# Performance work log

Hardware: AMD Instinct MI355X
Metric: run time of the kernel (lower is better)

## Reference

```python
import jax, jax.numpy as jnp
import numpy as np

N = 50000          # nodes
E = 800000         # edges per relation per prop step (avg degree 16)
NNZ = 1600000      # total sparse feature entries (32 per node)
IN_DIM = 20000     # feature vocab (EmbeddingBag rows)
H_DIM = 128        # hidden dim
OUT_DIM = 256      # GO label dim
HEADS = 1
LN_EPS = 1e-5


def _xn(k, shape, gain=1.0):
    fan_in, fan_out = shape[0], shape[-1]
    std = gain * np.sqrt(2.0 / (fan_in + fan_out))
    return std * jax.random.normal(k, shape, dtype=jnp.float32)


def setup_inputs() -> dict:
    key = jax.random.key(0)
    ks = jax.random.split(key, 32)
    d = {}
    d['emb_indices'] = jax.random.randint(ks[0], (NNZ,), 0, IN_DIM)
    d['emb_offsets'] = jnp.arange(N + 1) * (NNZ // N)  # include_last_offset=True
    d['emb_weights'] = jax.random.uniform(ks[1], (NNZ,), dtype=jnp.float32)
    d['y'] = jax.random.uniform(ks[2], (N, OUT_DIM), dtype=jnp.float32)
    d['flag'] = jax.random.randint(ks[3], (N,), 0, 2).astype(bool)
    for i, name in enumerate(['src_p1', 'dst_p1', 'src_s1', 'dst_s1',
                              'src_p2', 'dst_p2', 'src_s2', 'dst_s2']):
        d[name] = jax.random.randint(ks[4 + i], (E,), 0, N)
    g = np.sqrt(2.0)  # relu gain
    d['embed_W'] = _xn(ks[12], (IN_DIM, H_DIM))
    d['embed_b'] = jnp.zeros((H_DIM,), jnp.float32)
    d['mlp_W1'] = _xn(ks[13], (H_DIM, H_DIM)); d['mlp_b1'] = jnp.zeros((H_DIM,), jnp.float32)
    d['ln1_g'] = jnp.ones((H_DIM,), jnp.float32); d['ln1_b'] = jnp.zeros((H_DIM,), jnp.float32)
    d['mlp_W2'] = _xn(ks[14], (H_DIM, H_DIM)); d['mlp_b2'] = jnp.zeros((H_DIM,), jnp.float32)
    d['ln2_g'] = jnp.ones((H_DIM,), jnp.float32); d['ln2_b'] = jnp.zeros((H_DIM,), jnp.float32)
    d['Wsrc1'] = _xn(ks[15], (H_DIM, HEADS * H_DIM), g); d['bsrc1'] = jnp.zeros((HEADS * H_DIM,), jnp.float32)
    d['attn1'] = _xn(ks[16], (1, HEADS, H_DIM), g)
    d['Wsrc2'] = _xn(ks[17], (H_DIM, HEADS * H_DIM), g); d['bsrc2'] = jnp.zeros((HEADS * H_DIM,), jnp.float32)
    d['attn2'] = _xn(ks[18], (1, HEADS, H_DIM), g)
    d['out_W'] = _xn(ks[19], (H_DIM, OUT_DIM)); d['out_b'] = jnp.zeros((OUT_DIM,), jnp.float32)
    return d


def _layernorm(x, g, b):
    mu = jnp.mean(x, axis=-1, keepdims=True)
    var = jnp.mean((x - mu) ** 2, axis=-1, keepdims=True)
    return (x - mu) * jax.lax.rsqrt(var + LN_EPS) * g + b


def _edge_softmax(s, dst, n):
    # per-destination-node softmax over incoming edges, per head. s: (E, H)
    m = jax.ops.segment_max(s, dst, num_segments=n)
    ex = jnp.exp(s - m[dst])
    den = jax.ops.segment_sum(ex, dst, num_segments=n)
    return ex / den[dst]


def _gat(x, src, dst, W, b, attn, n):
    # block semantics: feat_dst = feat_src[:n_dst] (fc_dst unused in DGL block path)
    f = (x @ W + b).reshape(n, HEADS, -1)            # (N, H, F)
    e = jax.nn.leaky_relu(f[src] + f[dst], 0.2)       # u_add_v, (E, H, F)
    s = jnp.sum(e * attn, axis=-1)                    # (E, H)
    a = _edge_softmax(s, dst, n)                      # (E, H)
    rst = jax.ops.segment_sum(f[src] * a[:, :, None], dst, num_segments=n)  # (N,H,F)
    rst = rst + x[:, None, :]  # Identity residual (heads=1, in_dim == out_feats)
    return rst.mean(axis=1), a.mean(axis=1)           # (N, F), (E,)


def _prop(x, y, flag, src_p, dst_p, src_s, dst_s, W, b, attn, n):
    h_p, a_p = _gat(x, src_p, dst_p, W, b, attn, n)
    h_s, a_s = _gat(x, src_s, dst_s, W, b, attn, n)
    h = jax.nn.elu(h_p + h_s)
    # label propagation: u_mul_e with the (averaged) attention coefficients
    y_i = jax.ops.segment_sum(y[src_p] * a_p[:, None], dst_p, num_segments=n)
    y_s = jax.ops.segment_sum(y[src_s] * a_s[:, None], dst_s, num_segments=n)
    yh = y_i + y_s
    yh = yh / jnp.maximum(jnp.linalg.norm(yh, axis=1, keepdims=True), 1e-12)  # F.normalize
    yh = jnp.where(flag[:, None], y, yh)  # y_hat[dst_flag] = y0
    return h, yh


def reference(emb_indices, emb_offsets, emb_weights, y, flag,
              src_p1, dst_p1, src_s1, dst_s1, src_p2, dst_p2, src_s2, dst_s2,
              embed_W, embed_b, mlp_W1, mlp_b1, ln1_g, ln1_b,
              mlp_W2, mlp_b2, ln2_g, ln2_b,
              Wsrc1, bsrc1, attn1, Wsrc2, bsrc2, attn2, out_W, out_b):
    n = emb_offsets.shape[0] - 1
    nnz = emb_indices.shape[0]
    # EmbeddingBag(mode='sum', per_sample_weights, include_last_offset=True)
    seg = jnp.searchsorted(emb_offsets, jnp.arange(nnz), side='right') - 1
    h = jax.ops.segment_sum(embed_W[emb_indices] * emb_weights[:, None], seg, num_segments=n)
    h = jax.nn.relu(h + embed_b)
    # MLP: (Linear -> LayerNorm -> ReLU) x 2, dropout=0 (eval)
    h = jax.nn.relu(_layernorm(h @ mlp_W1 + mlp_b1, ln1_g, ln1_b))
    h = jax.nn.relu(_layernorm(h @ mlp_W2 + mlp_b2, ln2_g, ln2_b))
    h, yh = _prop(h, y, flag, src_p1, dst_p1, src_s1, dst_s1, Wsrc1, bsrc1, attn1, n)
    h, yh = _prop(h, yh, flag, src_p2, dst_p2, src_s2, dst_s2, Wsrc2, bsrc2, attn2, n)
    return h @ out_W + out_b, yh
```

## Files before the change

kernel.cpp:

```cpp
#include <hip/hip_runtime.h>
#include <hip/hip_bf16.h>

using bf16 = __hip_bfloat16;

#define HD 128
#define OD 256
#define NPASS 8

__device__ __forceinline__ float bl(unsigned lo){ return __uint_as_float(lo << 16); }
__device__ __forceinline__ float bh(unsigned u){ return __uint_as_float(u & 0xffff0000u); }

__device__ __forceinline__ void loadw4(const float* W, size_t off, float* w){
  float4 v = *(const float4*)(W + off); w[0]=v.x; w[1]=v.y; w[2]=v.z; w[3]=v.w;
}
__device__ __forceinline__ void loadw4(const bf16* W, size_t off, float* w){
  uint2 v = *(const uint2*)(W + off);
  w[0]=bl(v.x); w[1]=bh(v.x); w[2]=bl(v.y); w[3]=bh(v.y);
}

__global__ void k_detect(const void* __restrict__ w, int* __restrict__ dflag){
  if (threadIdx.x != 0 || blockIdx.x != 0) return;
  const bf16* p = (const bf16*)w;
  int f32 = 0;
  for (int i = 0; i < 128; ++i){
    float v = (float)p[i];
    if (!(v >= -0.001f && v <= 1.001f)) { f32 = 1; break; }
  }
  *dflag = f32;
}

__global__ void k_pack(const void* __restrict__ src, bf16* __restrict__ dst,
                       int n, const int* __restrict__ dflag){
  int i = blockIdx.x*blockDim.x + threadIdx.x;
  if (i >= n) return;
  float v = *dflag ? ((const float*)src)[i] : (float)((const bf16*)src)[i];
  dst[i] = (bf16)v;
}

__global__ void k_zero(int* __restrict__ p, int n){
  int i = blockIdx.x*blockDim.x + threadIdx.x;
  if (i < n) p[i] = 0;
}
__global__ void k_count4(const int* __restrict__ d0, const int* __restrict__ d1,
                         const int* __restrict__ d2, const int* __restrict__ d3,
                         int e0, int e1, int e2, int e3,
                         int* __restrict__ deg4, int N){
  int r = blockIdx.y;
  const int* dst = (r==0)?d0:(r==1)?d1:(r==2)?d2:d3;
  int E = (r==0)?e0:(r==1)?e1:(r==2)?e2:e3;
  int e = blockIdx.x*blockDim.x + threadIdx.x;
  if (e < E) atomicAdd(&deg4[r*N + dst[e]], 1);
}
__global__ void k_scan4(const int* __restrict__ deg4, int* __restrict__ rs4,
                        int* __restrict__ cur4, int N){
  const int T = 1024;
  __shared__ int lds[T];
  int r = blockIdx.x;
  const int* deg = deg4 + (size_t)r*N;
  int* rs  = rs4 + (size_t)r*(N+1);
  int* cur = cur4 + (size_t)r*N;
  int t = threadIdx.x;
  int chunk = (N + T - 1) / T;
  int a = t*chunk, b = min(N, a + chunk);
  int s = 0;
  for (int i = a; i < b; ++i) s += deg[i];
  lds[t] = s; __syncthreads();
  for (int o = 1; o < T; o <<= 1){
    int x = (t >= o) ? lds[t-o] : 0;
    __syncthreads();
    lds[t] += x;
    __syncthreads();
  }
  int run = (t > 0) ? lds[t-1] : 0;
  for (int i = a; i < b; ++i){ rs[i] = run; cur[i] = run; run += deg[i]; }
  if (t == T-1) rs[N] = lds[T-1];
}
__global__ void k_scatter4(const int* __restrict__ s0, const int* __restrict__ d0,
                           const int* __restrict__ s1, const int* __restrict__ d1,
                           const int* __restrict__ s2, const int* __restrict__ d2,
                           const int* __restrict__ s3, const int* __restrict__ d3,
                           int e0, int e1, int e2, int e3,
                           int* __restrict__ cur4, int* __restrict__ csr4,
                           int N, int Emax){
  int r = blockIdx.y;
  int pass = blockIdx.z;
  const int* src = (r==0)?s0:(r==1)?s1:(r==2)?s2:s3;
  const int* dst = (r==0)?d0:(r==1)?d1:(r==2)?d2:d3;
  int E = (r==0)?e0:(r==1)?e1:(r==2)?e2:e3;
  int e = blockIdx.x*blockDim.x + threadIdx.x;
  if (e >= E) return;
  int d = dst[e];
  int chunk = (N + NPASS - 1) / NPASS;
  int lo = pass * chunk;
  if (d < lo || d >= lo + chunk) return;
  int pos = atomicAdd(&cur4[r*N + d], 1);
  csr4[(size_t)r*Emax + pos] = src[e];
}

__global__ __launch_bounds__(128)
void k_embed(const int* __restrict__ idx, const int* __restrict__ off,
             const void* __restrict__ w, const bf16* __restrict__ Wb,
             const void* __restrict__ bias, float* __restrict__ h,
             int N, const int* __restrict__ dflag)
{
  int i = blockIdx.x; if (i >= N) return;
  int t = threadIdx.x;
  int wave = t >> 6;
  int g = (t >> 4) & 3;
  int st = wave*4 + g;
  int l16 = t & 15;

  __shared__ float se[2][HD];

  int isf32 = *dflag;
  int s0 = off[i], s1 = off[i+1];

  const uint4* W4 = (const uint4*)Wb;

  float acc[8];
  #pragma unroll
  for (int k = 0; k < 8; ++k) acc[k] = 0.f;

  for (int j = s0 + st; j < s1; j += 8){
    int u = idx[j];
    float wj = isf32 ? ((const float*)w)[j] : (float)((const bf16*)w)[j];
    uint4 f4 = W4[(size_t)u*16 + l16];
    float fu[8];
    fu[0]=bl(f4.x); fu[1]=bh(f4.x); fu[2]=bl(f4.y); fu[3]=bh(f4.y);
    fu[4]=bl(f4.z); fu[5]=bh(f4.z); fu[6]=bl(f4.w); fu[7]=bh(f4.w);
    #pragma unroll
    for (int k = 0; k < 8; ++k) acc[k] = fmaf(wj, fu[k], acc[k]);
  }

  #pragma unroll
  for (int k = 0; k < 8; ++k){
    acc[k] += __shfl_xor(acc[k], 16);
    acc[k] += __shfl_xor(acc[k], 32);
  }
  if (g == 0){
    *(float4*)&se[wave][8*l16]     = make_float4(acc[0],acc[1],acc[2],acc[3]);
    *(float4*)&se[wave][8*l16 + 4] = make_float4(acc[4],acc[5],acc[6],acc[7]);
  }
  __syncthreads();

  float b = isf32 ? ((const float*)bias)[t] : (float)((const bf16*)bias)[t];
  float val = se[0][t] + se[1][t] + b;
  h[(size_t)i*HD + t] = fmaxf(val, 0.f);
}

#define LBM 64
template<typename T>
__device__ __forceinline__ void linear_tiled_body(const float* __restrict__ x, const T* __restrict__ W,
    const T* __restrict__ b, const T* __restrict__ g, const T* __restrict__ bb,
    float* __restrict__ outf, bf16* __restrict__ outb, int do_ln, int do_relu, int N,
    float* __restrict__ xs)
{
  int t = threadIdx.x;
  int row0 = blockIdx.x * LBM;

  {
    int rl = t >> 2;
    int k0 = (t & 3) * 32;
    int gr = row0 + rl;
    if (gr < N){
      const float4* xr = (const float4*)(x + (size_t)gr*HD + k0);
      #pragma unroll
      for (int i = 0; i < 8; ++i){
        float4 v = xr[i];
        int k = k0 + i*4;
        xs[(k+0)*LBM + rl] = v.x;
        xs[(k+1)*LBM + rl] = v.y;
        xs[(k+2)*LBM + rl] = v.z;
        xs[(k+3)*LBM + rl] = v.w;
      }
    } else {
      #pragma unroll
      for (int i = 0; i < 32; ++i) xs[(k0+i)*LBM + rl] = 0.f;
    }
  }
  __syncthreads();

  int q = t & 31;
  int gidx = t >> 5;
  int c0 = q * 4;
  int rbase = gidx * 8;

  float bias4[4];
  loadw4(b, c0, bias4);

  float acc[8][4];
  #pragma unroll
  for (int i = 0; i < 8; ++i)
    #pragma unroll
    for (int j = 0; j < 4; ++j) acc[i][j] = bias4[j];

  #pragma unroll 4
  for (int k = 0; k < HD; ++k){
    float w4[4];
    loadw4(W, (size_t)k*HD + c0, w4);
    float4 xa = *(const float4*)&xs[k*LBM + rbase];
    float4 xb = *(const float4*)&xs[k*LBM + rbase + 4];
    float xv[8] = {xa.x, xa.y, xa.z, xa.w, xb.x, xb.y, xb.z, xb.w};
    #pragma unroll
    for (int i = 0; i < 8; ++i){
      acc[i][0] = fmaf(xv[i], w4[0], acc[i][0]);
      acc[i][1] = fmaf(xv[i], w4[1], acc[i][1]);
      acc[i][2] = fmaf(xv[i], w4[2], acc[i][2]);
      acc[i][3] = fmaf(xv[i], w4[3], acc[i][3]);
    }
  }

  if (do_ln){
    float g4[4], bb4[4];
    loadw4(g, c0, g4);
    loadw4(bb, c0, bb4);
    #pragma unroll
    for (int i = 0; i < 8; ++i){
      float s = acc[i][0]+acc[i][1]+acc[i][2]+acc[i][3];
      s += __shfl_xor(s,1); s += __shfl_xor(s,2); s += __shfl_xor(s,4);
      s += __shfl_xor(s,8); s += __shfl_xor(s,16);
      float mu = s * (1.f/HD);
      float c0_ = acc[i][0]-mu, c1_ = acc[i][1]-mu, c2_ = acc[i][2]-mu, c3_ = acc[i][3]-mu;
      float v = c0_*c0_ + c1_*c1_ + c2_*c2_ + c3_*c3_;
      v += __shfl_xor(v,1); v += __shfl_xor(v,2); v += __shfl_xor(v,4);
      v += __shfl_xor(v,8); v += __shfl_xor(v,16);
      float inv = rsqrtf(v*(1.f/HD) + 1e-5f);
      acc[i][0] = c0_*inv*g4[0] + bb4[0];
      acc[i][1] = c1_*inv*g4[1] + bb4[1];
      acc[i][2] = c2_*inv*g4[2] + bb4[2];
      acc[i][3] = c3_*inv*g4[3] + bb4[3];
    }
  }
  if (do_relu){
    #pragma unroll
    for (int i = 0; i < 8; ++i)
      #pragma unroll
      for (int j = 0; j < 4; ++j) acc[i][j] = fmaxf(acc[i][j], 0.f);
  }

  #pragma unroll
  for (int i = 0; i < 8; ++i){
    int gr = row0 + rbase + i;
    if (gr >= N) continue;
    if (outf){
      *(float4*)&outf[(size_t)gr*HD + c0] = make_float4(acc[i][0], acc[i][1], acc[i][2], acc[i][3]);
    } else {
      bf16 tmp[4] = {(bf16)acc[i][0], (bf16)acc[i][1], (bf16)acc[i][2], (bf16)acc[i][3]};
      *(uint2*)&outb[(size_t)gr*HD + c0] = *(const uint2*)tmp;
    }
  }
}
__global__ __launch_bounds__(256)
void k_linear_tiled(const float* x, const void* W, const void* b,
                    const void* g, const void* bb, float* outf, bf16* outb,
                    int do_ln, int do_relu, int N, const int* dflag)
{
  __shared__ float xs[HD*LBM];
  if (*dflag) linear_tiled_body<float>(x, (const float*)W, (const float*)b, (const float*)g, (const float*)bb, outf, outb, do_ln, do_relu, N, xs);
  else        linear_tiled_body<bf16 >(x, (const bf16*)W,  (const bf16*)b,  (const bf16*)g,  (const bf16*)bb,  outf, outb, do_ln, do_relu, N, xs);
}

__global__ __launch_bounds__(128)
void k_fprop(const int* __restrict__ rs_p, const int* __restrict__ cs_p,
             const int* __restrict__ rs_s, const int* __restrict__ cs_s,
             const bf16* __restrict__ fb, const void* __restrict__ attn,
             float* __restrict__ h, const bf16* __restrict__ yin,
             const int* __restrict__ flag,
             bf16* __restrict__ yh_out_b, float* __restrict__ yh_out_f,
             int N, const int* __restrict__ dflag)
{
  int v = blockIdx.x;
  int t = threadIdx.x;
  int wave = t >> 6, lane = t & 63;
  int g = lane >> 4;
  int l16 = lane & 15;

  __shared__ __align__(16) float sr[2][HD];
  __shared__ __align__(16) float sy[2][OD];
  __shared__ float red[HD];

  int isf32 = *dflag;

  float av[8];
  #pragma unroll
  for (int k = 0; k < 8; ++k)
    av[k] = isf32 ? ((const float*)attn)[8*l16 + k]
                  : (float)((const bf16*)attn)[8*l16 + k];

  const uint4* fb4 = (const uint4*)fb;
  const uint4* yb4 = (const uint4*)yin;

  uint4 fv4 = fb4[(size_t)v*16 + l16];
  float fv[8];
  fv[0]=bl(fv4.x); fv[1]=bh(fv4.x); fv[2]=bl(fv4.y); fv[3]=bh(fv4.y);
  fv[4]=bl(fv4.z); fv[5]=bh(fv4.z); fv[6]=bl(fv4.w); fv[7]=bh(fv4.w);

  const int* rs = wave ? rs_s : rs_p;
  const int* cs = wave ? cs_s : cs_p;
  int a = rs[v], b = rs[v+1];

  float l = 0.f;
  float r[8], ya[16];
  #pragma unroll
  for (int k = 0; k < 8; ++k) r[k] = 0.f;
  #pragma unroll
  for (int k = 0; k < 16; ++k) ya[k] = 0.f;

  int j = a + g;
  int u = (j < b) ? cs[j] : 0;
  for (; j < b; j += 4){
    int jn = j + 4;
    int un = cs[(jn < b) ? jn : j];
    uint4 fu4 = fb4[(size_t)u*16 + l16];
    uint4 yu0 = yb4[(size_t)u*32 + l16];
    uint4 yu1 = yb4[(size_t)u*32 + 16 + l16];

    float fu[8];
    fu[0]=bl(fu4.x); fu[1]=bh(fu4.x); fu[2]=bl(fu4.y); fu[3]=bh(fu4.y);
    fu[4]=bl(fu4.z); fu[5]=bh(fu4.z); fu[6]=bl(fu4.w); fu[7]=bh(fu4.w);

    float p = 0.f;
    #pragma unroll
    for (int k = 0; k < 8; ++k){
      float s = fv[k] + fu[k];
      s = fmaxf(s, 0.2f*s);
      p = fmaf(s, av[k], p);
    }
    p += __shfl_xor(p, 1);
    p += __shfl_xor(p, 2);
    p += __shfl_xor(p, 4);
    p += __shfl_xor(p, 8);

    float w = __expf(fminf(p, 80.f));
    l += w;
    #pragma unroll
    for (int k = 0; k < 8; ++k) r[k] = fmaf(w, fu[k], r[k]);

    float yu[16];
    yu[0]=bl(yu0.x);  yu[1]=bh(yu0.x);  yu[2]=bl(yu0.y);  yu[3]=bh(yu0.y);
    yu[4]=bl(yu0.z);  yu[5]=bh(yu0.z);  yu[6]=bl(yu0.w);  yu[7]=bh(yu0.w);
    yu[8]=bl(yu1.x);  yu[9]=bh(yu1.x);  yu[10]=bl(yu1.y); yu[11]=bh(yu1.y);
    yu[12]=bl(yu1.z); yu[13]=bh(yu1.z); yu[14]=bl(yu1.w); yu[15]=bh(yu1.w);
    #pragma unroll
    for (int k = 0; k < 16; ++k) ya[k] = fmaf(w, yu[k], ya[k]);

    u = un;
  }

  #pragma unroll
  for (int k = 0; k < 8; ++k){
    r[k] += __shfl_xor(r[k], 16);
    r[k] += __shfl_xor(r[k], 32);
  }
  #pragma unroll
  for (int k = 0; k < 16; ++k){
    ya[k] += __shfl_xor(ya[k], 16);
    ya[k] += __shfl_xor(ya[k], 32);
  }
  l += __shfl_xor(l, 16);
  l += __shfl_xor(l, 32);
  float inv = (l > 0.f) ? 1.f/l : 0.f;

  if (g == 0){
    *(float4*)&sr[wave][8*l16]       = make_float4(r[0]*inv, r[1]*inv, r[2]*inv, r[3]*inv);
    *(float4*)&sr[wave][8*l16+4]     = make_float4(r[4]*inv, r[5]*inv, r[6]*inv, r[7]*inv);
    *(float4*)&sy[wave][8*l16]       = make_float4(ya[0]*inv, ya[1]*inv, ya[2]*inv, ya[3]*inv);
    *(float4*)&sy[wave][8*l16+4]     = make_float4(ya[4]*inv, ya[5]*inv, ya[6]*inv, ya[7]*inv);
    *(float4*)&sy[wave][HD+8*l16]    = make_float4(ya[8]*inv, ya[9]*inv, ya[10]*inv, ya[11]*inv);
    *(float4*)&sy[wave][HD+8*l16+4]  = make_float4(ya[12]*inv, ya[13]*inv, ya[14]*inv, ya[15]*inv);
  }
  __syncthreads();

  float hv = sr[0][t] + sr[1][t];
  float y0 = sy[0][t] + sy[1][t];
  float y1 = sy[0][t+HD] + sy[1][t+HD];

  float x = hv + 2.f*h[(size_t)v*HD + t];
  h[(size_t)v*HD + t] = (x > 0.f) ? x : expm1f(x);

  red[t] = y0*y0 + y1*y1;
  __syncthreads();
  for (int s = 64; s > 0; s >>= 1){ if (t < s) red[t] += red[t+s]; __syncthreads(); }
  float inv2 = 1.f / fmaxf(sqrtf(red[0]), 1e-12f);
  float o0, o1;
  if (flag[v]){
    o0 = (float)yin[(size_t)v*OD + t];
    o1 = (float)yin[(size_t)v*OD + t + HD];
  } else {
    o0 = y0*inv2; o1 = y1*inv2;
  }
  if (yh_out_b){
    yh_out_b[(size_t)v*OD + t]      = (bf16)o0;
    yh_out_b[(size_t)v*OD + t + HD] = (bf16)o1;
  } else {
    yh_out_f[(size_t)v*OD + t]      = o0;
    yh_out_f[(size_t)v*OD + t + HD] = o1;
  }
}

#define OBM 32
template<typename T, typename TW>
__device__ __forceinline__ void out_tiled_body(const float* __restrict__ h, const TW* __restrict__ W,
    const TW* __restrict__ bias, T* __restrict__ out, int N, float* __restrict__ xs)
{
  int t = threadIdx.x;
  int row0 = blockIdx.x * OBM;

  {
    int rl = t >> 3;
    int k0 = (t & 7) * 16;
    int gr = row0 + rl;
    if (gr < N){
      const float4* xr = (const float4*)(h + (size_t)gr*HD + k0);
      #pragma unroll
      for (int i = 0; i < 4; ++i){
        float4 v = xr[i];
        int k = k0 + i*4;
        xs[(k+0)*OBM + rl] = v.x;
        xs[(k+1)*OBM + rl] = v.y;
        xs[(k+2)*OBM + rl] = v.z;
        xs[(k+3)*OBM + rl] = v.w;
      }
    } else {
      #pragma unroll
      for (int i = 0; i < 16; ++i) xs[(k0+i)*OBM + rl] = 0.f;
    }
  }
  __syncthreads();

  int q = t & 63;
  int gidx = t >> 6;
  int c0 = q * 4;
  int rbase = gidx * 8;

  float bias4[4];
  loadw4(bias, c0, bias4);

  float acc[8][4];
  #pragma unroll
  for (int i = 0; i < 8; ++i)
    #pragma unroll
    for (int j = 0; j < 4; ++j) acc[i][j] = bias4[j];

  #pragma unroll 4
  for (int k = 0; k < HD; ++k){
    float w4[4];
    loadw4(W, (size_t)k*OD + c0, w4);
    float4 xa = *(const float4*)&xs[k*OBM + rbase];
    float4 xb = *(const float4*)&xs[k*OBM + rbase + 4];
    float xv[8] = {xa.x, xa.y, xa.z, xa.w, xb.x, xb.y, xb.z, xb.w};
    #pragma unroll
    for (int i = 0; i < 8; ++i){
      acc[i][0] = fmaf(xv[i], w4[0], acc[i][0]);
      acc[i][1] = fmaf(xv[i], w4[1], acc[i][1]);
      acc[i][2] = fmaf(xv[i], w4[2], acc[i][2]);
      acc[i][3] = fmaf(xv[i], w4[3], acc[i][3]);
    }
  }

  #pragma unroll
  for (int i = 0; i < 8; ++i){
    int gr = row0 + rbase + i;
    if (gr >= N) continue;
    T* o = out + (size_t)gr*OD + c0;
    o[0] = (T)acc[i][0]; o[1] = (T)acc[i][1]; o[2] = (T)acc[i][2]; o[3] = (T)acc[i][3];
  }
}
template<typename T>
__global__ __launch_bounds__(256)
void k_out_tiled(const float* h, const void* W, const void* bias, T* out, int N, const int* dflag)
{
  __shared__ float xs[HD*OBM];
  if (*dflag) out_tiled_body<T,float>(h, (const float*)W, (const float*)bias, out, N, xs);
  else        out_tiled_body<T,bf16 >(h, (const bf16*)W,  (const bf16*)bias,  out, N, xs);
}

extern "C" void kernel_launch(void* const* d_in, const int* in_sizes, int n_in,
                              void* d_out, int out_size, void* d_ws, size_t ws_size,
                              hipStream_t stream)
{
  const int*  emb_indices = (const int*)d_in[0];
  const int*  emb_offsets = (const int*)d_in[1];
  const void* emb_weights = d_in[2];
  const void* y           = d_in[3];
  const int*  flag        = (const int*)d_in[4];
  const int*  src_p1=(const int*)d_in[5],  *dst_p1=(const int*)d_in[6];
  const int*  src_s1=(const int*)d_in[7],  *dst_s1=(const int*)d_in[8];
  const int*  src_p2=(const int*)d_in[9],  *dst_p2=(const int*)d_in[10];
  const int*  src_s2=(const int*)d_in[11], *dst_s2=(const int*)d_in[12];
  const void* embed_W=d_in[13], *embed_b=d_in[14];
  const void* mlp_W1 =d_in[15], *mlp_b1 =d_in[16];
  const void* ln1_g  =d_in[17], *ln1_b  =d_in[18];
  const void* mlp_W2 =d_in[19], *mlp_b2 =d_in[20];
  const void* ln2_g  =d_in[21], *ln2_b  =d_in[22];
  const void* Wsrc1  =d_in[23], *bsrc1  =d_in[24], *attn1=d_in[25];
  const void* Wsrc2  =d_in[26], *bsrc2  =d_in[27], *attn2=d_in[28];
  const void* out_W  =d_in[29], *out_b  =d_in[30];

  int N   = in_sizes[1] - 1;
  int E1p = in_sizes[5], E1s = in_sizes[7], E2p = in_sizes[9], E2s = in_sizes[11];
  int Emax = max(max(E1p, E1s), max(E2p, E2s));
  int IN_DIM = in_sizes[13] / HD;

  long long elsz = (long long)out_size / ((long long)2*N*OD);

  float* ws = (float*)d_ws;
  float* h    = ws;  ws += (size_t)N*HD;
  bf16* fb    = (bf16*)ws; ws += (size_t)N*HD/2;
  bf16* yb    = (bf16*)ws; ws += (size_t)N*OD/2;
  bf16* yh1b  = (bf16*)ws; ws += (size_t)N*OD/2;
  bf16* Wb    = (bf16*)ws; ws += ((size_t)IN_DIM*HD + 1)/2;
  int* rs4    = (int*)ws; ws += 4*((size_t)N+1);
  int* csr4   = (int*)ws; ws += 4*(size_t)Emax;
  int* deg4   = (int*)ws; ws += 4*(size_t)N;
  int* cur4   = (int*)ws; ws += 4*(size_t)N;
  int* dflag  = (int*)ws; ws += 1;

  k_detect<<<1, 64, 0, stream>>>(emb_weights, dflag);

  k_pack<<<((size_t)IN_DIM*HD + 255)/256, 256, 0, stream>>>(embed_W, Wb, IN_DIM*HD, dflag);
  k_pack<<<((size_t)N*OD + 255)/256, 256, 0, stream>>>(y, yb, N*OD, dflag);

  dim3 cg((Emax + 255)/256, 4);
  dim3 sg((Emax + 255)/256, 4, NPASS);
  k_zero   <<<(4*N + 255)/256, 256, 0, stream>>>(deg4, 4*N);
  k_count4 <<<cg, 256, 0, stream>>>(dst_p1, dst_s1, dst_p2, dst_s2, E1p, E1s, E2p, E2s, deg4, N);
  k_scan4  <<<4, 1024, 0, stream>>>(deg4, rs4, cur4, N);
  k_scatter4<<<sg, 256, 0, stream>>>(src_p1, dst_p1, src_s1, dst_s1, src_p2, dst_p2, src_s2, dst_s2,
                                     E1p, E1s, E2p, E2s, cur4, csr4, N, Emax);
  int* rs_p1 = rs4;              int* cs_p1 = csr4;
  int* rs_s1 = rs4 + (N+1);      int* cs_s1 = csr4 + (size_t)Emax;
  int* rs_p2 = rs4 + 2*(N+1);    int* cs_p2 = csr4 + 2*(size_t)Emax;
  int* rs_s2 = rs4 + 3*(N+1);    int* cs_s2 = csr4 + 3*(size_t)Emax;

  int LG = (N + LBM - 1) / LBM;
  int OG = (N + OBM - 1) / OBM;

  k_embed<<<N, 128, 0, stream>>>(emb_indices, emb_offsets, emb_weights, Wb, embed_b, h, N, dflag);
  k_linear_tiled<<<LG, 256, 0, stream>>>(h, mlp_W1, mlp_b1, ln1_g, ln1_b, h, nullptr, 1, 1, N, dflag);
  k_linear_tiled<<<LG, 256, 0, stream>>>(h, mlp_W2, mlp_b2, ln2_g, ln2_b, h, nullptr, 1, 1, N, dflag);

  k_linear_tiled<<<LG, 256, 0, stream>>>(h, Wsrc1, bsrc1, nullptr, nullptr, nullptr, fb, 0, 0, N, dflag);
  k_fprop<<<N, 128, 0, stream>>>(rs_p1, cs_p1, rs_s1, cs_s1, fb, attn1, h, yb, flag, yh1b, nullptr, N, dflag);

  k_linear_tiled<<<LG, 256, 0, stream>>>(h, Wsrc2, bsrc2, nullptr, nullptr, nullptr, fb, 0, 0, N, dflag);
  if (elsz == 2){
    k_fprop<<<N, 128, 0, stream>>>(rs_p2, cs_p2, rs_s2, cs_s2, fb, attn2, h, yh1b, flag,
                                   (bf16*)d_out + (size_t)N*OD, nullptr, N, dflag);
    k_out_tiled<bf16><<<OG, 256, 0, stream>>>(h, out_W, out_b, (bf16*)d_out, N, dflag);
  } else {
    k_fprop<<<N, 128, 0, stream>>>(rs_p2, cs_p2, rs_s2, cs_s2, fb, attn2, h, yh1b, flag,
                                   nullptr, (float*)d_out + (size_t)N*OD, N, dflag);
    k_out_tiled<float><<<OG, 256, 0, stream>>>(h, out_W, out_b, (float*)d_out, N, dflag);
  }
}
```

Before: 1.239 ms.

## Double threads per node in embed and fprop kernels with two-deep gather unroll

The embedding-bag and attention-propagation kernels now use 256 threads per node instead of 128. The embed kernel runs 16 concurrent entry streams reduced through four shared partials. The fprop kernel assigns two waves per relation and processes two neighbors per iteration to raise memory-level parallelism. Its epilogue replaces the tree reduction in shared memory with wave shuffles and defers softmax normalization until after combining waves. With only about 16 neighbors and 32 entries per node, the wider blocks risk idle lanes and more block overhead.

```diff
diff --git a/kernel.cpp b/kernel.cpp
--- a/kernel.cpp
+++ b/kernel.cpp
@@ -97,7 +97,7 @@
   csr4[(size_t)r*Emax + pos] = src[e];
 }
 
-__global__ __launch_bounds__(128)
+__global__ __launch_bounds__(256)
 void k_embed(const int* __restrict__ idx, const int* __restrict__ off,
              const void* __restrict__ w, const bf16* __restrict__ Wb,
              const void* __restrict__ bias, float* __restrict__ h,
@@ -106,11 +106,10 @@
   int i = blockIdx.x; if (i >= N) return;
   int t = threadIdx.x;
   int wave = t >> 6;
-  int g = (t >> 4) & 3;
-  int st = wave*4 + g;
+  int st = t >> 4;
   int l16 = t & 15;
 
-  __shared__ float se[2][HD];
+  __shared__ float se[4][HD];
 
   int isf32 = *dflag;
   int s0 = off[i], s1 = off[i+1];
@@ -121,7 +120,7 @@
   #pragma unroll
   for (int k = 0; k < 8; ++k) acc[k] = 0.f;
 
-  for (int j = s0 + st; j < s1; j += 8){
+  for (int j = s0 + st; j < s1; j += 16){
     int u = idx[j];
     float wj = isf32 ? ((const float*)w)[j] : (float)((const bf16*)w)[j];
     uint4 f4 = W4[(size_t)u*16 + l16];
@@ -137,15 +136,17 @@
     acc[k] += __shfl_xor(acc[k], 16);
     acc[k] += __shfl_xor(acc[k], 32);
   }
-  if (g == 0){
+  if ((t & 0x30) == 0){
     *(float4*)&se[wave][8*l16]     = make_float4(acc[0],acc[1],acc[2],acc[3]);
     *(float4*)&se[wave][8*l16 + 4] = make_float4(acc[4],acc[5],acc[6],acc[7]);
   }
   __syncthreads();
 
-  float b = isf32 ? ((const float*)bias)[t] : (float)((const bf16*)bias)[t];
-  float val = se[0][t] + se[1][t] + b;
-  h[(size_t)i*HD + t] = fmaxf(val, 0.f);
+  if (t < HD){
+    float b = isf32 ? ((const float*)bias)[t] : (float)((const bf16*)bias)[t];
+    float val = se[0][t] + se[1][t] + se[2][t] + se[3][t] + b;
+    h[(size_t)i*HD + t] = fmaxf(val, 0.f);
+  }
 }
 
 #define LBM 64
@@ -260,7 +261,7 @@
   else        linear_tiled_body<bf16 >(x, (const bf16*)W,  (const bf16*)b,  (const bf16*)g,  (const bf16*)bb,  outf, outb, do_ln, do_relu, N, xs);
 }
 
-__global__ __launch_bounds__(128)
+__global__ __launch_bounds__(256)
 void k_fprop(const int* __restrict__ rs_p, const int* __restrict__ cs_p,
              const int* __restrict__ rs_s, const int* __restrict__ cs_s,
              const bf16* __restrict__ fb, const void* __restrict__ attn,
@@ -271,13 +272,16 @@
 {
   int v = blockIdx.x;
   int t = threadIdx.x;
-  int wave = t >> 6, lane = t & 63;
-  int g = lane >> 4;
-  int l16 = lane & 15;
-
-  __shared__ __align__(16) float sr[2][HD];
-  __shared__ __align__(16) float sy[2][OD];
-  __shared__ float red[HD];
+  int wave = t >> 6;
+  int rel  = wave >> 1;
+  int lane = t & 63;
+  int gg   = ((wave & 1) << 2) | (lane >> 4);
+  int l16  = lane & 15;
+
+  __shared__ float sl[4];
+  __shared__ __align__(16) float sr[4][HD];
+  __shared__ __align__(16) float sy[4][OD];
+  __shared__ float sq[4];
 
   int isf32 = *dflag;
 
@@ -295,8 +299,8 @@
   fv[0]=bl(fv4.x); fv[1]=bh(fv4.x); fv[2]=bl(fv4.y); fv[3]=bh(fv4.y);
   fv[4]=bl(fv4.z); fv[5]=bh(fv4.z); fv[6]=bl(fv4.w); fv[7]=bh(fv4.w);
 
-  const int* rs = wave ? rs_s : rs_p;
-  const int* cs = wave ? cs_s : cs_p;
+  const int* rs = rel ? rs_s : rs_p;
+  const int* cs = rel ? cs_s : cs_p;
   int a = rs[v], b = rs[v+1];
 
   float l = 0.f;
@@ -306,45 +310,72 @@
   #pragma unroll
   for (int k = 0; k < 16; ++k) ya[k] = 0.f;
 
-  int j = a + g;
-  int u = (j < b) ? cs[j] : 0;
-  for (; j < b; j += 4){
-    int jn = j + 4;
-    int un = cs[(jn < b) ? jn : j];
-    uint4 fu4 = fb4[(size_t)u*16 + l16];
-    uint4 yu0 = yb4[(size_t)u*32 + l16];
-    uint4 yu1 = yb4[(size_t)u*32 + 16 + l16];
-
-    float fu[8];
-    fu[0]=bl(fu4.x); fu[1]=bh(fu4.x); fu[2]=bl(fu4.y); fu[3]=bh(fu4.y);
-    fu[4]=bl(fu4.z); fu[5]=bh(fu4.z); fu[6]=bl(fu4.w); fu[7]=bh(fu4.w);
-
-    float p = 0.f;
-    #pragma unroll
-    for (int k = 0; k < 8; ++k){
-      float s = fv[k] + fu[k];
-      s = fmaxf(s, 0.2f*s);
-      p = fmaf(s, av[k], p);
-    }
-    p += __shfl_xor(p, 1);
-    p += __shfl_xor(p, 2);
-    p += __shfl_xor(p, 4);
-    p += __shfl_xor(p, 8);
-
-    float w = __expf(fminf(p, 80.f));
-    l += w;
-    #pragma unroll
-    for (int k = 0; k < 8; ++k) r[k] = fmaf(w, fu[k], r[k]);
-
-    float yu[16];
-    yu[0]=bl(yu0.x);  yu[1]=bh(yu0.x);  yu[2]=bl(yu0.y);  yu[3]=bh(yu0.y);
-    yu[4]=bl(yu0.z);  yu[5]=bh(yu0.z);  yu[6]=bl(yu0.w);  yu[7]=bh(yu0.w);
-    yu[8]=bl(yu1.x);  yu[9]=bh(yu1.x);  yu[10]=bl(yu1.y); yu[11]=bh(yu1.y);
-    yu[12]=bl(yu1.z); yu[13]=bh(yu1.z); yu[14]=bl(yu1.w); yu[15]=bh(yu1.w);
-    #pragma unroll
-    for (int k = 0; k < 16; ++k) ya[k] = fmaf(w, yu[k], ya[k]);
-
-    u = un;
+  for (int j = a + gg; j < b; j += 16){
+    int j1 = j + 8;
+    int u0 = cs[j];
+    int u1 = cs[(j1 < b) ? j1 : j];
+    uint4 f0  = fb4[(size_t)u0*16 + l16];
+    uint4 y00 = yb4[(size_t)u0*32 + l16];
+    uint4 y01 = yb4[(size_t)u0*32 + 16 + l16];
+    uint4 f1  = fb4[(size_t)u1*16 + l16];
+    uint4 y10 = yb4[(size_t)u1*32 + l16];
+    uint4 y11 = yb4[(size_t)u1*32 + 16 + l16];
+
+    {
+      float fu[8];
+      fu[0]=bl(f0.x); fu[1]=bh(f0.x); fu[2]=bl(f0.y); fu[3]=bh(f0.y);
+      fu[4]=bl(f0.z); fu[5]=bh(f0.z); fu[6]=bl(f0.w); fu[7]=bh(f0.w);
+      float p = 0.f;
+      #pragma unroll
+      for (int k = 0; k < 8; ++k){
+        float s = fv[k] + fu[k];
+        s = fmaxf(s, 0.2f*s);
+        p = fmaf(s, av[k], p);
+      }
+      p += __shfl_xor(p, 1);
+      p += __shfl_xor(p, 2);
+      p += __shfl_xor(p, 4);
+      p += __shfl_xor(p, 8);
+      float w = __expf(fminf(p, 80.f));
+      l += w;
+      #pragma unroll
+      for (int k = 0; k < 8; ++k) r[k] = fmaf(w, fu[k], r[k]);
+      float yu[16];
+      yu[0]=bl(y00.x);  yu[1]=bh(y00.x);  yu[2]=bl(y00.y);  yu[3]=bh(y00.y);
+      yu[4]=bl(y00.z);  yu[5]=bh(y00.z);  yu[6]=bl(y00.w);  yu[7]=bh(y00.w);
+      yu[8]=bl(y01.x);  yu[9]=bh(y01.x);  yu[10]=bl(y01.y); yu[11]=bh(y01.y);
+      yu[12]=bl(y01.z); yu[13]=bh(y01.z); yu[14]=bl(y01.w); yu[15]=bh(y01.w);
+      #pragma unroll
+      for (int k = 0; k < 16; ++k) ya[k] = fmaf(w, yu[k], ya[k]);
+    }
+
+    if (j1 < b){
+      float fu[8];
+      fu[0]=bl(f1.x); fu[1]=bh(f1.x); fu[2]=bl(f1.y); fu[3]=bh(f1.y);
+      fu[4]=bl(f1.z); fu[5]=bh(f1.z); fu[6]=bl(f1.w); fu[7]=bh(f1.w);
+      float p = 0.f;
+      #pragma unroll
+      for (int k = 0; k < 8; ++k){
+        float s = fv[k] + fu[k];
+        s = fmaxf(s, 0.2f*s);
+        p = fmaf(s, av[k], p);
+      }
+      p += __shfl_xor(p, 1);
+      p += __shfl_xor(p, 2);
+      p += __shfl_xor(p, 4);
+      p += __shfl_xor(p, 8);
+      float w = __expf(fminf(p, 80.f));
+      l += w;
+      #pragma unroll
+      for (int k = 0; k < 8; ++k) r[k] = fmaf(w, fu[k], r[k]);
+      float yu[16];
+      yu[0]=bl(y10.x);  yu[1]=bh(y10.x);  yu[2]=bl(y10.y);  yu[3]=bh(y10.y);
+      yu[4]=bl(y10.z);  yu[5]=bh(y10.z);  yu[6]=bl(y10.w);  yu[7]=bh(y10.w);
+      yu[8]=bl(y11.x);  yu[9]=bh(y11.x);  yu[10]=bl(y11.y); yu[11]=bh(y11.y);
+      yu[12]=bl(y11.z); yu[13]=bh(y11.z); yu[14]=bl(y11.w); yu[15]=bh(y11.w);
+      #pragma unroll
+      for (int k = 0; k < 16; ++k) ya[k] = fmaf(w, yu[k], ya[k]);
+    }
   }
 
   #pragma unroll
@@ -359,43 +390,42 @@
   }
   l += __shfl_xor(l, 16);
   l += __shfl_xor(l, 32);
-  float inv = (l > 0.f) ? 1.f/l : 0.f;
-
-  if (g == 0){
-    *(float4*)&sr[wave][8*l16]       = make_float4(r[0]*inv, r[1]*inv, r[2]*inv, r[3]*inv);
-    *(float4*)&sr[wave][8*l16+4]     = make_float4(r[4]*inv, r[5]*inv, r[6]*inv, r[7]*inv);
-    *(float4*)&sy[wave][8*l16]       = make_float4(ya[0]*inv, ya[1]*inv, ya[2]*inv, ya[3]*inv);
-    *(float4*)&sy[wave][8*l16+4]     = make_float4(ya[4]*inv, ya[5]*inv, ya[6]*inv, ya[7]*inv);
-    *(float4*)&sy[wave][HD+8*l16]    = make_float4(ya[8]*inv, ya[9]*inv, ya[10]*inv, ya[11]*inv);
-    *(float4*)&sy[wave][HD+8*l16+4]  = make_float4(ya[12]*inv, ya[13]*inv, ya[14]*inv, ya[15]*inv);
+
+  if (lane < 16){
+    *(float4*)&sr[wave][8*l16]       = make_float4(r[0], r[1], r[2], r[3]);
+    *(float4*)&sr[wave][8*l16+4]     = make_float4(r[4], r[5], r[6], r[7]);
+    *(float4*)&sy[wave][8*l16]       = make_float4(ya[0], ya[1], ya[2], ya[3]);
+    *(float4*)&sy[wave][8*l16+4]     = make_float4(ya[4], ya[5], ya[6], ya[7]);
+    *(float4*)&sy[wave][HD+8*l16]    = make_float4(ya[8], ya[9], ya[10], ya[11]);
+    *(float4*)&sy[wave][HD+8*l16+4]  = make_float4(ya[12], ya[13], ya[14], ya[15]);
+    if (l16 == 0) sl[wave] = l;
   }
   __syncthreads();
 
-  float hv = sr[0][t] + sr[1][t];
-  float y0 = sy[0][t] + sy[1][t];
-  float y1 = sy[0][t+HD] + sy[1][t+HD];
-
-  float x = hv + 2.f*h[(size_t)v*HD + t];
-  h[(size_t)v*HD + t] = (x > 0.f) ? x : expm1f(x);
-
-  red[t] = y0*y0 + y1*y1;
+  float Lp = sl[0] + sl[1];
+  float Ls = sl[2] + sl[3];
+  float invp = (Lp > 0.f) ? 1.f/Lp : 0.f;
+  float invs = (Ls > 0.f) ? 1.f/Ls : 0.f;
+
+  if (t < HD){
+    float hv = (sr[0][t] + sr[1][t])*invp + (sr[2][t] + sr[3][t])*invs;
+    float x = hv + 2.f*h[(size_t)v*HD + t];
+    h[(size_t)v*HD + t] = (x > 0.f) ? x : expm1f(x);
+  }
+
+  float yv = (sy[0][t] + sy[1][t])*invp + (sy[2][t] + sy[3][t])*invs;
+
+  float q = yv*yv;
+  q += __shfl_xor(q, 1);  q += __shfl_xor(q, 2);  q += __shfl_xor(q, 4);
+  q += __shfl_xor(q, 8);  q += __shfl_xor(q, 16); q += __shfl_xor(q, 32);
+  if (lane == 0) sq[wave] = q;
   __syncthreads();
-  for (int s = 64; s > 0; s >>= 1){ if (t < s) red[t] += red[t+s]; __syncthreads(); }
-  float inv2 = 1.f / fmaxf(sqrtf(red[0]), 1e-12f);
-  float o0, o1;
-  if (flag[v]){
-    o0 = (float)yin[(size_t)v*OD + t];
-    o1 = (float)yin[(size_t)v*OD + t + HD];
-  } else {
-    o0 = y0*inv2; o1 = y1*inv2;
-  }
-  if (yh_out_b){
-    yh_out_b[(size_t)v*OD + t]      = (bf16)o0;
-    yh_out_b[(size_t)v*OD + t + HD] = (bf16)o1;
-  } else {
-    yh_out_f[(size_t)v*OD + t]      = o0;
-    yh_out_f[(size_t)v*OD + t + HD] = o1;
-  }
+  float nrm2 = sq[0] + sq[1] + sq[2] + sq[3];
+  float inv2 = 1.f / fmaxf(sqrtf(nrm2), 1e-12f);
+
+  float o = flag[v] ? (float)yin[(size_t)v*OD + t] : yv*inv2;
+  if (yh_out_b) yh_out_b[(size_t)v*OD + t] = (bf16)o;
+  else          yh_out_f[(size_t)v*OD + t] = o;
 }
 
 #define OBM 32
@@ -536,20 +566,20 @@
   int LG = (N + LBM - 1) / LBM;
   int OG = (N + OBM - 1) / OBM;
 
-  k_embed<<<N, 128, 0, stream>>>(emb_indices, emb_offsets, emb_weights, Wb, embed_b, h, N, dflag);
+  k_embed<<<N, 256, 0, stream>>>(emb_indices, emb_offsets, emb_weights, Wb, embed_b, h, N, dflag);
   k_linear_tiled<<<LG, 256, 0, stream>>>(h, mlp_W1, mlp_b1, ln1_g, ln1_b, h, nullptr, 1, 1, N, dflag);
   k_linear_tiled<<<LG, 256, 0, stream>>>(h, mlp_W2, mlp_b2, ln2_g, ln2_b, h, nullptr, 1, 1, N, dflag);
 
   k_linear_tiled<<<LG, 256, 0, stream>>>(h, Wsrc1, bsrc1, nullptr, nullptr, nullptr, fb, 0, 0, N, dflag);
-  k_fprop<<<N, 128, 0, stream>>>(rs_p1, cs_p1, rs_s1, cs_s1, fb, attn1, h, yb, flag, yh1b, nullptr, N, dflag);
+  k_fprop<<<N, 256, 0, stream>>>(rs_p1, cs_p1, rs_s1, cs_s1, fb, attn1, h, yb, flag, yh1b, nullptr, N, dflag);
 
   k_linear_tiled<<<LG, 256, 0, stream>>>(h, Wsrc2, bsrc2, nullptr, nullptr, nullptr, fb, 0, 0, N, dflag);
   if (elsz == 2){
-    k_fprop<<<N, 128, 0, stream>>>(rs_p2, cs_p2, rs_s2, cs_s2, fb, attn2, h, yh1b, flag,
+    k_fprop<<<N, 256, 0, stream>>>(rs_p2, cs_p2, rs_s2, cs_s2, fb, attn2, h, yh1b, flag,
                                    (bf16*)d_out + (size_t)N*OD, nullptr, N, dflag);
     k_out_tiled<bf16><<<OG, 256, 0, stream>>>(h, out_W, out_b, (bf16*)d_out, N, dflag);
   } else {
-    k_fprop<<<N, 128, 0, stream>>>(rs_p2, cs_p2, rs_s2, cs_s2, fb, attn2, h, yh1b, flag,
+    k_fprop<<<N, 256, 0, stream>>>(rs_p2, cs_p2, rs_s2, cs_s2, fb, attn2, h, yh1b, flag,
                                    nullptr, (float*)d_out + (size_t)N*OD, N, dflag);
     k_out_tiled<float><<<OG, 256, 0, stream>>>(h, out_W, out_b, (float*)d_out, N, dflag);
   }
```

New measurement: 1.541 ms. 1.24x slower.
